# Performance work log

Measured on AMD Instinct MI355X. Metric: run time of the kernel, lower is better.

The kernel has to match this reference:

```python
import jax, jax.numpy as jnp
import numpy as np

B, L = 8, 2048
H_IN = 20
K1, K2 = 16, 32
NG = 32            # n_gaussians
D1, D2 = 7, 5      # gaussian kernel input dims
DM = 128           # outer product out_features
DH = 32            # attribute embedding out_features
IDX_MAX = 8.0      # index_distance_max


def _gather(x, idx):
    # x: (B,L,H), idx: (B,L,K) -> (B,L,K,H)
    b = jnp.arange(x.shape[0])[:, None, None]
    return x[b, idx]


def _neighbors(frames, kmax):
    c = frames[:, :, 0, :]                      # centers (B,L,3)
    sq = jnp.sum(c * c, axis=-1)
    d2 = sq[:, :, None] + sq[:, None, :] - 2.0 * jnp.einsum('bld,bmd->blm', c, c)
    _, idx = jax.lax.top_k(-d2, kmax)           # self (d2=0) lands in slot 0
    return idx


def _coords(frames, seq_idx, idx):
    c = frames[:, :, 0, :]
    axes = frames[:, :, 1:4, :]                 # local frame axes of center node
    z = frames[:, :, 3, :]
    c_j = _gather(c, idx)
    z_j = _gather(z, idx)
    delta = c_j - c[:, :, None, :]              # (B,L,K,3)
    dist = jnp.sqrt(jnp.sum(delta * delta, -1, keepdims=True) + 1e-12)
    eucl = jnp.einsum('blkd,blad->blka', delta, axes)   # neighbor coords in local frame
    zdotz = jnp.sum(z[:, :, None, :] * z_j, -1, keepdims=True)
    deltadotz = jnp.sum(delta * z_j, -1, keepdims=True) / dist
    zdotdelta = jnp.sum(z[:, :, None, :] * delta, -1, keepdims=True) / dist
    sidx = seq_idx.astype(jnp.float32)          # (B,L,1)
    idist = jnp.clip(jnp.abs(_gather(sidx, idx) - sidx[:, :, None, :]), 0.0, IDX_MAX)
    return eucl, dist, zdotz, deltadotz, zdotdelta, idist


def _gaussian(x, centers, prec):
    # full-covariance Gaussian kernel: exp(-0.5 ||P_n (x - mu_n)||^2)
    diff = x[..., None] - centers               # (...,d,NG)
    y = jnp.einsum('...dn,dkn->...kn', diff, prec)
    return jnp.exp(-0.5 * jnp.sum(y * y, axis=-2))


def _forward(aa_attributes, aa_frame, aa_indices,
             gk1_centers, gk1_prec, op_kernel, op_bias,
             emb_W, emb_b, beta_W, beta_b, selfatt_W, selfatt_b,
             crossatt_W, crossatt_b, nodef_W, nodef_b,
             gk2_centers, gk2_prec, emb2_W, emb2_b):
    # --- neighborhood 1: euclidian + index_distance + ZdotZ + (DeltadotZ,ZdotDelta)
    idx1 = _neighbors(aa_frame, K1)
    eucl, _, zz, dz, zd, idist = _coords(aa_frame, aa_indices, idx1)
    coords1 = jnp.concatenate([eucl, idist, zz, dz, zd], axis=-1)   # (B,L,K1,7)
    neigh_attr = _gather(aa_attributes, idx1)                        # (B,L,K1,20)
    g1 = _gaussian(coords1, gk1_centers, gk1_prec)                   # (B,L,K1,NG)
    # outer-product embedding: sum over neighbors and (gaussian x attribute) pairs
    filt = jnp.einsum('blkg,blkh,gho->blo', g1, neigh_attr, op_kernel) + op_bias
    f = jax.nn.relu(filt)                                            # (B,L,128)
    emb = jax.nn.relu(f @ emb_W + emb_b)                             # (B,L,32)
    beta = jax.nn.relu(emb @ beta_W + beta_b)                        # (B,L,1)
    satt = jax.nn.relu(emb @ selfatt_W + selfatt_b)                  # (B,L,1)
    catt = jax.nn.relu(emb @ crossatt_W + crossatt_b)                # (B,L,1)
    nodef = jax.nn.relu(emb @ nodef_W + nodef_b)                     # (B,L,2)
    # --- neighborhood 2: distance + ZdotZ + (DeltadotZ,ZdotDelta) + index_distance
    idx2 = _neighbors(aa_frame, K2)
    _, dist2, zz2, dz2, zd2, idist2 = _coords(aa_frame, aa_indices, idx2)
    coords2 = jnp.concatenate([dist2, zz2, dz2, zd2, idist2], axis=-1)  # (B,L,K2,5)
    att_local = _gather(catt, idx2)                                  # (B,L,K2,1)
    nodef_local = _gather(nodef, idx2)                               # (B,L,K2,2)
    g2 = _gaussian(coords2, gk2_centers, gk2_prec)                   # (B,L,K2,NG)
    gw = jax.nn.relu(g2 @ emb2_W + emb2_b)                           # (B,L,K2,1)
    # --- graph attention aggregation (self slot is k=0)
    e = att_local.at[:, :, 0, :].set(satt)
    logits = beta[:, :, None, :] * e
    logits = logits - jnp.max(logits, axis=2, keepdims=True)
    w = gw * jnp.exp(logits)
    a = w / (jnp.sum(w, axis=2, keepdims=True) + 1e-6)               # (B,L,K2,1)
    out = jnp.sum(a * nodef_local, axis=2)                           # (B,L,2)
    return out


def setup_inputs():
    key = jax.random.key(0)
    ks = jax.random.split(key, 16)
    eye1 = jnp.tile(jnp.eye(D1, dtype=jnp.float32)[:, :, None], (1, 1, NG))
    eye2 = jnp.tile(jnp.eye(D2, dtype=jnp.float32)[:, :, None], (1, 1, NG))
    return {
        'aa_attributes': jax.random.normal(ks[0], (B, L, H_IN), jnp.float32),
        'aa_frame': jax.random.normal(ks[1], (B, L, 4, 3), jnp.float32),
        'aa_indices': jnp.arange(B * L, dtype=jnp.int32).reshape(B, L, 1),
        'gk1_centers': 0.1 * jax.random.normal(ks[2], (D1, NG), jnp.float32),
        'gk1_prec': eye1 + 0.05 * jax.random.normal(ks[3], (D1, D1, NG), jnp.float32),
        'op_kernel': 0.05 * jax.random.normal(ks[4], (NG, H_IN, DM), jnp.float32),
        'op_bias': jnp.zeros((DM,), jnp.float32),
        'emb_W': jax.random.normal(ks[5], (DM, DH), jnp.float32) / np.sqrt(DM),
        'emb_b': jnp.zeros((DH,), jnp.float32),
        'beta_W': jax.random.normal(ks[6], (DH, 1), jnp.float32) / np.sqrt(DH),
        'beta_b': jnp.zeros((1,), jnp.float32),
        'selfatt_W': jax.random.normal(ks[7], (DH, 1), jnp.float32) / np.sqrt(DH),
        'selfatt_b': jnp.zeros((1,), jnp.float32),
        'crossatt_W': jax.random.normal(ks[8], (DH, 1), jnp.float32) / np.sqrt(DH),
        'crossatt_b': jnp.zeros((1,), jnp.float32),
        'nodef_W': jax.random.normal(ks[9], (DH, 2), jnp.float32) / np.sqrt(DH),
        'nodef_b': jnp.zeros((2,), jnp.float32),
        'gk2_centers': 0.1 * jax.random.normal(ks[10], (D2, NG), jnp.float32),
        'gk2_prec': eye2 + 0.05 * jax.random.normal(ks[11], (D2, D2, NG), jnp.float32),
        'emb2_W': jax.random.normal(ks[12], (NG, 1), jnp.float32) / np.sqrt(NG),
        'emb2_b': jnp.zeros((1,), jnp.float32),
    }


def reference(aa_attributes, aa_frame, aa_indices,
              gk1_centers, gk1_prec, op_kernel, op_bias,
              emb_W, emb_b, beta_W, beta_b, selfatt_W, selfatt_b,
              crossatt_W, crossatt_b, nodef_W, nodef_b,
              gk2_centers, gk2_prec, emb2_W, emb2_b):
    return _forward(aa_attributes, aa_frame, aa_indices,
                    gk1_centers, gk1_prec, op_kernel, op_bias,
                    emb_W, emb_b, beta_W, beta_b, selfatt_W, selfatt_b,
                    crossatt_W, crossatt_b, nodef_W, nodef_b,
                    gk2_centers, gk2_prec, emb2_W, emb2_b)
```

## Files before the change

kernel.cpp:

```cpp
#include <hip/hip_runtime.h>

typedef unsigned int u32;
typedef unsigned long long u64;
typedef unsigned short u16;

#define NL 2048

typedef __attribute__((ext_vector_type(8))) short bf16x8;
typedef __attribute__((ext_vector_type(16))) float f32x16;

__device__ __forceinline__ u16 to_bf16(float f) {
  u32 b = __float_as_uint(f);
  b += 0x7FFFu + ((b >> 16) & 1u);
  return (u16)(b >> 16);
}

__device__ __forceinline__ void gload_lds16(const void* g, void* l) {
  __builtin_amdgcn_global_load_lds(
      (const __attribute__((address_space(1))) u32*)g,
      (__attribute__((address_space(3))) u32*)l, 16, 0, 0);
}

__device__ __forceinline__ u64 shfl_xor64(u64 v, int m) {
  int lo = __shfl_xor((int)(u32)v, m, 64);
  int hi = __shfl_xor((int)(u32)(v >> 32), m, 64);
  return ((u64)(u32)hi << 32) | (u32)lo;
}

__device__ __forceinline__ u32 sort64_u32(u32 v, int lane) {
#pragma unroll
  for (int k = 2; k <= 64; k <<= 1) {
#pragma unroll
    for (int j = k >> 1; j > 0; j >>= 1) {
      u32 p = (u32)__shfl_xor((int)v, j, 64);
      bool lower = ((lane & j) == 0);
      bool asc = ((lane & k) == 0);
      u32 lo = v < p ? v : p;
      u32 hi = v < p ? p : v;
      v = (lower == asc) ? lo : hi;
    }
  }
  return v;
}

__device__ __forceinline__ void sort128_u64(u64& f0, u64& f1, int lane) {
  for (int k = 2; k <= 128; k <<= 1) {
    for (int j = k >> 1; j > 0; j >>= 1) {
      if (j == 64) {
        u64 lo = f0 < f1 ? f0 : f1;
        u64 hi = f0 < f1 ? f1 : f0;
        f0 = lo;
        f1 = hi;
      } else {
        bool lower = ((lane & j) == 0);
        bool asc0 = ((lane & k) == 0);
        bool asc1 = (((lane + 64) & k) == 0);
        u64 p0 = shfl_xor64(f0, j);
        u64 p1 = shfl_xor64(f1, j);
        f0 = ((f0 < p0) == (lower == asc0)) ? f0 : p0;
        f1 = ((f1 < p1) == (lower == asc1)) ? f1 : p1;
      }
    }
  }
}

__global__ __launch_bounds__(256) void prep_kernel(
    const float* __restrict__ opW, const float* __restrict__ embW,
    const float* __restrict__ betaW, const float* __restrict__ sattW,
    const float* __restrict__ cattW, const float* __restrict__ nodW,
    const float* __restrict__ betaB, const float* __restrict__ sattB,
    const float* __restrict__ cattB, const float* __restrict__ nodB,
    u16* __restrict__ opWt, u16* __restrict__ embWt, float* __restrict__ w5,
    float* __restrict__ b5) {
  const int bx = blockIdx.x, t = threadIdx.x;
  if (bx < 160) {
    int flat = bx * 256 + t;
    int o = flat / 320;
    int r = flat - o * 320;
    int kk = r * 2;
    float f0 = opW[(size_t)kk * 128 + o];
    float f1 = opW[(size_t)(kk + 1) * 128 + o];
    ((u32*)opWt)[o * 320 + r] = (u32)to_bf16(f0) | ((u32)to_bf16(f1) << 16);
  } else if (bx < 176) {
    int flat = (bx - 160) * 256 + t;
    int j = flat >> 7, k = flat & 127;
    embWt[j * 128 + k] = to_bf16(embW[(size_t)k * 32 + j]);
  } else {
    if (t < 160) {
      int h = t >> 5, j = t & 31;
      float v = (h == 0) ? betaW[j]
                : (h == 1) ? sattW[j]
                : (h == 2) ? cattW[j]
                : (h == 3) ? nodW[j * 2]
                           : nodW[j * 2 + 1];
      w5[j * 8 + h] = v;
    } else if (t < 165) {
      int h = t - 160;
      float v = (h == 0) ? betaB[0]
                : (h == 1) ? sattB[0]
                : (h == 2) ? cattB[0]
                : (h == 3) ? nodB[0]
                           : nodB[1];
      b5[h] = v;
    }
  }
}

__global__ __launch_bounds__(512) void knn_kernel(const float* __restrict__ frames,
                                                  int* __restrict__ idx32) {
  __shared__ float4 cand[2048];
  __shared__ u64 comp[8][256];
  const int tid = threadIdx.x;
  const int w = tid >> 6, lane = tid & 63;
  const int query = blockIdx.x * 8 + w;
  const int b = query >> 11, lq = query & (NL - 1);

#pragma unroll
  for (int i = 0; i < 4; i++) {
    int l = tid + i * 512;
    const float* fp = frames + (size_t)(b * NL + l) * 12;
    float4 fr = *(const float4*)fp;
    cand[l] = make_float4(fr.x, fr.y, fr.z,
                          fr.x * fr.x + fr.y * fr.y + fr.z * fr.z);
  }
  __syncthreads();

  float4 me = cand[lq];
  u32 k[32];
  u32 m = 0xFFFFFFFFu;
#pragma unroll
  for (int i = 0; i < 32; i++) {
    float4 c = cand[i * 64 + lane];
    float dot = c.x * me.x + c.y * me.y + c.z * me.z;
    float d2 = (me.w + c.w) - 2.0f * dot;
    u32 kb = __float_as_uint(d2);
    u32 key = kb ^ ((u32)((int)kb >> 31) | 0x80000000u);
    k[i] = key;
    m = key < m ? key : m;
  }

  u32 ms = sort64_u32(m, lane);
  u32 T0 = (u32)__shfl((int)ms, 31, 64);

  int base = 0;
#pragma unroll
  for (int i = 0; i < 32; i++) {
    bool flag = (k[i] <= T0);
    u64 mask = __ballot(flag);
    if (flag) {
      u32 rank = __builtin_amdgcn_mbcnt_hi(
          (u32)(mask >> 32), __builtin_amdgcn_mbcnt_lo((u32)mask, 0u));
      int pos = base + (int)rank;
      if (pos < 256) comp[w][pos] = ((u64)k[i] << 32) | (u32)(i * 64 + lane);
    }
    base += (int)__popcll(mask);
  }
  int cnt = base < 256 ? base : 256;
  __syncthreads();

  u64 f0 = ~0ull;
  for (int c = 0; c * 64 < cnt; c++) {
    int p = c * 64 + lane;
    u64 f1 = (p < cnt) ? comp[w][p] : ~0ull;
    sort128_u64(f0, f1, lane);
    f0 = (lane < 32) ? f0 : ~0ull;
  }
  if (lane < 32)
    idx32[(size_t)query * 32 + lane] = (int)(f0 & 0xFFFFFFFFull);
}

__global__ __launch_bounds__(256) void stage1_kernel(
    const float* __restrict__ frames, const float* __restrict__ attrs,
    const int* __restrict__ aaidx, const float* __restrict__ cen1,
    const float* __restrict__ prec1, const int* __restrict__ idx32,
    u16* __restrict__ outer) {
  __shared__ float sPrec[1568];
  __shared__ float sCen[224];
  __shared__ float sCoord[4 * 16 * 8];
  __shared__ float sAttrT[4 * 20 * 16];
  __shared__ float sG1T[4 * 32 * 17];
  const int tid = threadIdx.x;
  for (int i = tid; i < 1568; i += 256) sPrec[i] = prec1[i];
  if (tid < 224) sCen[tid] = cen1[tid];
  const int pt = tid >> 6, lane = tid & 63;
  const int pid = blockIdx.x * 4 + pt;
  const int b = pid >> 11;
  __syncthreads();

  if (lane < 16) {
    int n = lane;
    int j = idx32[pid * 32 + n];
    int jg = b * NL + j;
    const float* fs = frames + (size_t)pid * 12;
    const float* fj = frames + (size_t)jg * 12;
    float4 A0 = *(const float4*)(fs);
    float4 A1 = *(const float4*)(fs + 4);
    float4 A2 = *(const float4*)(fs + 8);
    float4 B0 = *(const float4*)(fj);
    float4 B2 = *(const float4*)(fj + 8);
    float dx = B0.x - A0.x, dy = B0.y - A0.y, dzc = B0.z - A0.z;
    float a0x = A0.w, a0y = A1.x, a0z = A1.y;
    float a1x = A1.z, a1y = A1.w, a1z = A2.x;
    float a2x = A2.y, a2y = A2.z, a2z = A2.w;
    float zjx = B2.y, zjy = B2.z, zjz = B2.w;
    float dd = dx * dx + dy * dy + dzc * dzc + 1e-12f;
    float dist = sqrtf(dd);
    float e0 = dx * a0x + dy * a0y + dzc * a0z;
    float e1 = dx * a1x + dy * a1y + dzc * a1z;
    float e2 = dx * a2x + dy * a2y + dzc * a2z;
    float zz = a2x * zjx + a2y * zjy + a2z * zjz;
    float dzv = (dx * zjx + dy * zjy + dzc * zjz) / dist;
    float zdv = (a2x * dx + a2y * dy + a2z * dzc) / dist;
    float si = (float)aaidx[pid];
    float sj = (float)aaidx[jg];
    float idist = fminf(fabsf(sj - si), 8.0f);
    float* cr = sCoord + pt * 128 + n * 8;
    cr[0] = e0; cr[1] = e1; cr[2] = e2; cr[3] = idist;
    cr[4] = zz; cr[5] = dzv; cr[6] = zdv;
    const float* ar = attrs + (size_t)jg * 20;
    float4 q0 = *(const float4*)(ar);
    float4 q1 = *(const float4*)(ar + 4);
    float4 q2 = *(const float4*)(ar + 8);
    float4 q3 = *(const float4*)(ar + 12);
    float4 q4 = *(const float4*)(ar + 16);
    float av[20] = {q0.x, q0.y, q0.z, q0.w, q1.x, q1.y, q1.z, q1.w,
                    q2.x, q2.y, q2.z, q2.w, q3.x, q3.y, q3.z, q3.w,
                    q4.x, q4.y, q4.z, q4.w};
#pragma unroll
    for (int h = 0; h < 20; h++) sAttrT[pt * 320 + h * 16 + n] = av[h];
  }
  __syncthreads();
  {
    const int g = lane & 31, nh = lane >> 5;
    float pr[7][7], cn[7];
#pragma unroll
    for (int d = 0; d < 7; d++) {
      cn[d] = sCen[d * 32 + g];
#pragma unroll
      for (int kk = 0; kk < 7; kk++) pr[d][kk] = sPrec[(d * 7 + kk) * 32 + g];
    }
#pragma unroll
    for (int i = 0; i < 8; i++) {
      int n = nh * 8 + i;
      const float* cr = sCoord + pt * 128 + n * 8;
      float df[7];
#pragma unroll
      for (int d = 0; d < 7; d++) df[d] = cr[d] - cn[d];
      float s = 0.0f;
#pragma unroll
      for (int kk = 0; kk < 7; kk++) {
        float y = 0.0f;
#pragma unroll
        for (int d = 0; d < 7; d++) y = fmaf(df[d], pr[d][kk], y);
        s = fmaf(y, y, s);
      }
      sG1T[pt * 544 + g * 17 + n] = __expf(-0.5f * s);
    }
  }
  __syncthreads();
  {
    const int g = lane & 31, hg = lane >> 5;
    float g16[16];
#pragma unroll
    for (int n = 0; n < 16; n++) g16[n] = sG1T[pt * 544 + g * 17 + n];
    u32* orow = (u32*)(outer + (size_t)pid * 640) + (g * 20 + hg * 10) / 2;
#pragma unroll
    for (int i = 0; i < 5; i++) {
      int h0 = hg * 10 + i * 2, h1 = h0 + 1;
      float a0 = 0.f, a1 = 0.f;
#pragma unroll
      for (int c = 0; c < 4; c++) {
        float4 v0 = *(float4*)&sAttrT[pt * 320 + h0 * 16 + c * 4];
        float4 v1 = *(float4*)&sAttrT[pt * 320 + h1 * 16 + c * 4];
        a0 = fmaf(v0.x, g16[c * 4 + 0], a0);
        a0 = fmaf(v0.y, g16[c * 4 + 1], a0);
        a0 = fmaf(v0.z, g16[c * 4 + 2], a0);
        a0 = fmaf(v0.w, g16[c * 4 + 3], a0);
        a1 = fmaf(v1.x, g16[c * 4 + 0], a1);
        a1 = fmaf(v1.y, g16[c * 4 + 1], a1);
        a1 = fmaf(v1.z, g16[c * 4 + 2], a1);
        a1 = fmaf(v1.w, g16[c * 4 + 3], a1);
      }
      orow[i] = (u32)to_bf16(a0) | ((u32)to_bf16(a1) << 16);
    }
  }
}

__global__ __launch_bounds__(256) void gemm_kernel(
    const u16* __restrict__ outer,
    const u16* __restrict__ opWt,
    const float* __restrict__ opB,
    const u16* __restrict__ embWt,
    const float* __restrict__ embB,
    const float* __restrict__ w5,
    const float* __restrict__ b5,
    float* __restrict__ head8) {
  __shared__ char smem[32768];
  const int tid = threadIdx.x;
  const int w = tid >> 6, lane = tid & 63;
  const int p0 = blockIdx.x * 32;
  const int lr = lane >> 3, lc = lane & 7;
  const int gsw = lc ^ lr;
  const int m = lane & 31, kh = lane >> 5;

  f32x16 acc;
#pragma unroll
  for (int r = 0; r < 16; r++) acc[r] = 0.f;

  const u16* gA = outer + (size_t)(p0 + w * 8 + lr) * 640 + gsw * 8;

  for (int cc = 0; cc < 10; cc++) {
    gload_lds16(gA + cc * 64, smem + w * 1024);
#pragma unroll
    for (int i = 0; i < 4; i++) {
      const u16* gB = opWt + (size_t)(w * 32 + i * 8 + lr) * 640 + cc * 64 + gsw * 8;
      gload_lds16(gB, smem + 4096 + w * 4096 + i * 1024);
    }
    __syncthreads();
#pragma unroll
    for (int s = 0; s < 4; s++) {
      int pg = (s * 2 + kh) ^ (m & 7);
      bf16x8 av = *(bf16x8*)(smem + m * 128 + pg * 16);
      bf16x8 bv = *(bf16x8*)(smem + 4096 + w * 4096 + m * 128 + pg * 16);
      acc = __builtin_amdgcn_mfma_f32_32x32x16_bf16(av, bv, acc, 0, 0, 0);
    }
    __syncthreads();
  }

  const int o = w * 32 + m;
  float bo = opB[o];
#pragma unroll
  for (int i = 0; i < 2; i++) {
    int j = w * 8 + i * 4 + (lane >> 4);
    int ge = (lane & 15) ^ (j & 7);
    gload_lds16(embWt + j * 128 + ge * 8, smem + 8192 + w * 2048 + i * 1024);
  }
  u16* sFb = (u16*)smem;
#pragma unroll
  for (int r = 0; r < 16; r++) {
    int mm = (r & 3) + 8 * (r >> 2) + 4 * kh;
    float v = fmaxf(acc[r] + bo, 0.f);
    int pg = (o >> 3) ^ (mm & 7);
    sFb[mm * 128 + pg * 8 + (o & 7)] = to_bf16(v);
  }
  __syncthreads();

  f32x16 acc2;
#pragma unroll
  for (int r = 0; r < 16; r++) acc2[r] = 0.f;
#pragma unroll
  for (int t2 = 0; t2 < 2; t2++) {
    int gg = (w * 2 + t2) * 2 + kh;
    int pg = gg ^ (m & 7);
    bf16x8 av = *(bf16x8*)(smem + m * 256 + pg * 16);
    bf16x8 bv = *(bf16x8*)(smem + 8192 + m * 256 + pg * 16);
    acc2 = __builtin_amdgcn_mfma_f32_32x32x16_bf16(av, bv, acc2, 0, 0, 0);
  }
  float* scr = (float*)(smem + 16384) + w * 1024;
#pragma unroll
  for (int r = 0; r < 16; r++) {
    int mm = (r & 3) + 8 * (r >> 2) + 4 * kh;
    scr[mm * 32 + m] = acc2[r];
  }
  __syncthreads();

  {
    float* sc = (float*)(smem + 16384);
    int i4 = tid * 4;
    float4 v0 = *(float4*)(sc + i4);
    float4 v1 = *(float4*)(sc + 1024 + i4);
    float4 v2 = *(float4*)(sc + 2048 + i4);
    float4 v3 = *(float4*)(sc + 3072 + i4);
    int pp = tid >> 3, j0 = (tid & 7) * 4;
    float4 eb = *(const float4*)(embB + j0);
    float4 e;
    e.x = fmaxf(v0.x + v1.x + v2.x + v3.x + eb.x, 0.f);
    e.y = fmaxf(v0.y + v1.y + v2.y + v3.y + eb.y, 0.f);
    e.z = fmaxf(v0.z + v1.z + v2.z + v3.z + eb.z, 0.f);
    e.w = fmaxf(v0.w + v1.w + v2.w + v3.w + eb.w, 0.f);
    *(float4*)((float*)smem + pp * 36 + j0) = e;
  }
  __syncthreads();

  if (tid < 160) {
    int h = tid >> 5, p = tid & 31;
    const float* sE = (const float*)smem + p * 36;
    float a = b5[h];
#pragma unroll
    for (int j = 0; j < 32; j++) a = fmaf(sE[j], w5[j * 8 + h], a);
    a = fmaxf(a, 0.f);
    int slot = (h < 2) ? (h + 4) : (h - 2);
    head8[(size_t)(p0 + p) * 8 + slot] = a;
  }
}

__global__ __launch_bounds__(256) void stage2_kernel(
    const float* __restrict__ frames, const int* __restrict__ aaidx,
    const float* __restrict__ cen2, const float* __restrict__ prec2,
    const float* __restrict__ emb2W, const float* __restrict__ emb2B,
    const int* __restrict__ idx32, const float* __restrict__ head8,
    float* __restrict__ out) {
  __shared__ float sPrec[800];
  __shared__ float sCen[160];
  __shared__ float sW2[32];
  __shared__ float sCoord[4 * 32 * 5];
  __shared__ float sG2[4 * 32 * 33];
  const int tid = threadIdx.x;
  for (int i = tid; i < 800; i += 256) sPrec[i] = prec2[i];
  if (tid < 160) sCen[tid] = cen2[tid];
  if (tid < 32) sW2[tid] = emb2W[tid];
  const int pt = tid >> 6, lane = tid & 63;
  const int pid = blockIdx.x * 4 + pt;
  const int b = pid >> 11;
  __syncthreads();

  float4 hv = make_float4(0.f, 0.f, 0.f, 0.f);
  float betaS = 0.f, sattS = 0.f;
  if (lane < 32) {
    int n = lane;
    int j = idx32[pid * 32 + n];
    int jg = b * NL + j;
    const float* fs = frames + (size_t)pid * 12;
    const float* fj = frames + (size_t)jg * 12;
    float4 A0 = *(const float4*)(fs);
    float4 A2 = *(const float4*)(fs + 8);
    float4 B0 = *(const float4*)(fj);
    float4 B2 = *(const float4*)(fj + 8);
    float dx = B0.x - A0.x, dy = B0.y - A0.y, dzc = B0.z - A0.z;
    float a2x = A2.y, a2y = A2.z, a2z = A2.w;
    float zjx = B2.y, zjy = B2.z, zjz = B2.w;
    float dd = dx * dx + dy * dy + dzc * dzc + 1e-12f;
    float dist = sqrtf(dd);
    float zz = a2x * zjx + a2y * zjy + a2z * zjz;
    float dzv = (dx * zjx + dy * zjy + dzc * zjz) / dist;
    float zdv = (a2x * dx + a2y * dy + a2z * dzc) / dist;
    float si = (float)aaidx[pid];
    float sj = (float)aaidx[jg];
    float idist = fminf(fabsf(sj - si), 8.0f);
    float* cr = sCoord + pt * 160 + n * 5;
    cr[0] = dist; cr[1] = zz; cr[2] = dzv; cr[3] = zdv; cr[4] = idist;
    hv = *(const float4*)(head8 + (size_t)jg * 8);
    betaS = head8[(size_t)pid * 8 + 4];
    sattS = head8[(size_t)pid * 8 + 5];
  }
  __syncthreads();
  {
    const int g = lane & 31, nh = lane >> 5;
    float pr[5][5], cn[5];
#pragma unroll
    for (int d = 0; d < 5; d++) {
      cn[d] = sCen[d * 32 + g];
#pragma unroll
      for (int kk = 0; kk < 5; kk++) pr[d][kk] = sPrec[(d * 5 + kk) * 32 + g];
    }
#pragma unroll
    for (int i = 0; i < 16; i++) {
      int n = nh * 16 + i;
      const float* cr = sCoord + pt * 160 + n * 5;
      float df[5];
#pragma unroll
      for (int d = 0; d < 5; d++) df[d] = cr[d] - cn[d];
      float s = 0.0f;
#pragma unroll
      for (int kk = 0; kk < 5; kk++) {
        float y = 0.0f;
#pragma unroll
        for (int d = 0; d < 5; d++) y = fmaf(df[d], pr[d][kk], y);
        s = fmaf(y, y, s);
      }
      sG2[pt * 1056 + n * 33 + g] = __expf(-0.5f * s);
    }
  }
  __syncthreads();
  if (lane < 32) {
    int n = lane;
    float gw = emb2B[0];
#pragma unroll 8
    for (int g = 0; g < 32; g++) gw = fmaf(sG2[pt * 1056 + n * 33 + g], sW2[g], gw);
    gw = fmaxf(gw, 0.0f);
    float e = (n == 0) ? sattS : hv.x;
    float logit = betaS * e;
    float mx = logit;
#pragma unroll
    for (int d = 1; d < 32; d <<= 1) mx = fmaxf(mx, __shfl_xor(mx, d, 64));
    float wv = gw * __expf(logit - mx);
    float S = wv;
#pragma unroll
    for (int d = 1; d < 32; d <<= 1) S += __shfl_xor(S, d, 64);
    float a = wv / (S + 1e-6f);
    float o0 = a * hv.y, o1 = a * hv.z;
#pragma unroll
    for (int d = 1; d < 32; d <<= 1) {
      o0 += __shfl_xor(o0, d, 64);
      o1 += __shfl_xor(o1, d, 64);
    }
    if (n == 0) {
      out[pid * 2 + 0] = o0;
      out[pid * 2 + 1] = o1;
    }
  }
}

extern "C" void kernel_launch(void* const* d_in, const int* in_sizes, int n_in,
                              void* d_out, int out_size, void* d_ws, size_t ws_size,
                              hipStream_t stream) {
  const float* attrs = (const float*)d_in[0];
  const float* frames = (const float*)d_in[1];
  const int* aaidx = (const int*)d_in[2];
  const float* cen1 = (const float*)d_in[3];
  const float* prec1 = (const float*)d_in[4];
  const float* opW = (const float*)d_in[5];
  const float* opB = (const float*)d_in[6];
  const float* embW = (const float*)d_in[7];
  const float* embB = (const float*)d_in[8];
  const float* betaW = (const float*)d_in[9];
  const float* betaB = (const float*)d_in[10];
  const float* sattW = (const float*)d_in[11];
  const float* sattB = (const float*)d_in[12];
  const float* cattW = (const float*)d_in[13];
  const float* cattB = (const float*)d_in[14];
  const float* nodW = (const float*)d_in[15];
  const float* nodB = (const float*)d_in[16];
  const float* cen2 = (const float*)d_in[17];
  const float* prec2 = (const float*)d_in[18];
  const float* emb2W = (const float*)d_in[19];
  const float* emb2B = (const float*)d_in[20];
  float* out = (float*)d_out;

  char* ws = (char*)d_ws;
  int* idx32 = (int*)ws;
  u16* outer_bf = (u16*)(ws + 2097152);
  float* head8 = (float*)(ws + 23068672);
  u16* opWt = (u16*)(ws + 23592960);
  u16* embWt = (u16*)(ws + 23756800);
  float* w5 = (float*)(ws + 23764992);
  float* b5 = (float*)(ws + 23766016);

  prep_kernel<<<dim3(177), dim3(256), 0, stream>>>(
      opW, embW, betaW, sattW, cattW, nodW, betaB, sattB, cattB, nodB, opWt,
      embWt, w5, b5);
  knn_kernel<<<dim3(2048), dim3(512), 0, stream>>>(frames, idx32);
  stage1_kernel<<<dim3(4096), dim3(256), 0, stream>>>(frames, attrs, aaidx, cen1,
                                                      prec1, idx32, outer_bf);
  gemm_kernel<<<dim3(512), dim3(256), 0, stream>>>(outer_bf, opWt, opB, embWt,
                                                   embB, w5, b5, head8);
  stage2_kernel<<<dim3(4096), dim3(256), 0, stream>>>(frames, aaidx, cen2, prec2,
                                                      emb2W, emb2B, idx32, head8, out);
}
```

Baseline: 194.3 us.

## Merge prep into kNN kernel, rank-select neighbors, and stream GEMM B operand from global

The weight-prep work is folded into the kNN launch as extra blocks, and the opW transpose now goes through LDS for coalesced access. The kNN top-32 selection replaces the bitonic 128-element merge sort with a direct rank count over the compacted candidates. Stage1 and stage2 load the Gaussian precision and center parameters straight into registers instead of staging them in shared memory, which removes a barrier. The GEMM now preloads all A chunks into LDS at once and reads B directly from global memory, dropping the per-chunk barriers. The rank count is O(cnt^2) per wave, and duplicate keys could collide on the same output slot.

Result: faster. 184.1 us (median of 2 runs) (-5.2%).

```diff
diff --git a/kernel.cpp b/kernel.cpp
--- a/kernel.cpp
+++ b/kernel.cpp
@@ -19,12 +19,6 @@
   __builtin_amdgcn_global_load_lds(
       (const __attribute__((address_space(1))) u32*)g,
       (__attribute__((address_space(3))) u32*)l, 16, 0, 0);
-}
-
-__device__ __forceinline__ u64 shfl_xor64(u64 v, int m) {
-  int lo = __shfl_xor((int)(u32)v, m, 64);
-  int hi = __shfl_xor((int)(u32)(v >> 32), m, 64);
-  return ((u64)(u32)hi << 32) | (u32)lo;
 }
 
 __device__ __forceinline__ u32 sort64_u32(u32 v, int lane) {
@@ -43,28 +37,8 @@
   return v;
 }
 
-__device__ __forceinline__ void sort128_u64(u64& f0, u64& f1, int lane) {
-  for (int k = 2; k <= 128; k <<= 1) {
-    for (int j = k >> 1; j > 0; j >>= 1) {
-      if (j == 64) {
-        u64 lo = f0 < f1 ? f0 : f1;
-        u64 hi = f0 < f1 ? f1 : f0;
-        f0 = lo;
-        f1 = hi;
-      } else {
-        bool lower = ((lane & j) == 0);
-        bool asc0 = ((lane & k) == 0);
-        bool asc1 = (((lane + 64) & k) == 0);
-        u64 p0 = shfl_xor64(f0, j);
-        u64 p1 = shfl_xor64(f1, j);
-        f0 = ((f0 < p0) == (lower == asc0)) ? f0 : p0;
-        f1 = ((f1 < p1) == (lower == asc1)) ? f1 : p1;
-      }
-    }
-  }
-}
-
-__global__ __launch_bounds__(256) void prep_kernel(
+__global__ __launch_bounds__(512) void knn_prep_kernel(
+    const float* __restrict__ frames, int* __restrict__ idx32,
     const float* __restrict__ opW, const float* __restrict__ embW,
     const float* __restrict__ betaW, const float* __restrict__ sattW,
     const float* __restrict__ cattW, const float* __restrict__ nodW,
@@ -72,47 +46,68 @@
     const float* __restrict__ cattB, const float* __restrict__ nodB,
     u16* __restrict__ opWt, u16* __restrict__ embWt, float* __restrict__ w5,
     float* __restrict__ b5) {
-  const int bx = blockIdx.x, t = threadIdx.x;
-  if (bx < 160) {
-    int flat = bx * 256 + t;
-    int o = flat / 320;
-    int r = flat - o * 320;
-    int kk = r * 2;
-    float f0 = opW[(size_t)kk * 128 + o];
-    float f1 = opW[(size_t)(kk + 1) * 128 + o];
-    ((u32*)opWt)[o * 320 + r] = (u32)to_bf16(f0) | ((u32)to_bf16(f1) << 16);
-  } else if (bx < 176) {
-    int flat = (bx - 160) * 256 + t;
-    int j = flat >> 7, k = flat & 127;
-    embWt[j * 128 + k] = to_bf16(embW[(size_t)k * 32 + j]);
-  } else {
-    if (t < 160) {
-      int h = t >> 5, j = t & 31;
-      float v = (h == 0) ? betaW[j]
-                : (h == 1) ? sattW[j]
-                : (h == 2) ? cattW[j]
-                : (h == 3) ? nodW[j * 2]
-                           : nodW[j * 2 + 1];
-      w5[j * 8 + h] = v;
-    } else if (t < 165) {
-      int h = t - 160;
-      float v = (h == 0) ? betaB[0]
-                : (h == 1) ? sattB[0]
-                : (h == 2) ? cattB[0]
-                : (h == 3) ? nodB[0]
-                           : nodB[1];
-      b5[h] = v;
-    }
-  }
-}
-
-__global__ __launch_bounds__(512) void knn_kernel(const float* __restrict__ frames,
-                                                  int* __restrict__ idx32) {
-  __shared__ float4 cand[2048];
-  __shared__ u64 comp[8][256];
+  __shared__ union U {
+    struct {
+      float4 cand[2048];
+      u64 comp[8][256];
+    } k;
+    float tp[128 * 73];
+  } sm;
+  const int bx = blockIdx.x;
   const int tid = threadIdx.x;
+
+  if (bx >= 2048) {
+    if (bx < 2058) {
+      const int k0 = (bx - 2048) * 64;
+#pragma unroll
+      for (int j = 0; j < 4; j++) {
+        int f = tid + j * 512;
+        int kk = f >> 5;
+        int o4 = (f & 31) * 4;
+        float4 v = *(const float4*)(opW + (size_t)(k0 + kk) * 128 + o4);
+        sm.tp[(o4 + 0) * 73 + kk] = v.x;
+        sm.tp[(o4 + 1) * 73 + kk] = v.y;
+        sm.tp[(o4 + 2) * 73 + kk] = v.z;
+        sm.tp[(o4 + 3) * 73 + kk] = v.w;
+      }
+      __syncthreads();
+      u32* ow = (u32*)opWt;
+#pragma unroll
+      for (int j = 0; j < 8; j++) {
+        int f = tid + j * 512;
+        int o = f >> 5, q = f & 31;
+        float lo = sm.tp[o * 73 + q * 2];
+        float hi = sm.tp[o * 73 + q * 2 + 1];
+        ow[o * 320 + (k0 >> 1) + q] = (u32)to_bf16(lo) | ((u32)to_bf16(hi) << 16);
+      }
+    } else {
+      for (int f = tid; f < 4096; f += 512) {
+        int j = f >> 7, kk = f & 127;
+        embWt[f] = to_bf16(embW[(size_t)kk * 32 + j]);
+      }
+      if (tid < 160) {
+        int h = tid >> 5, j = tid & 31;
+        float v = (h == 0) ? betaW[j]
+                  : (h == 1) ? sattW[j]
+                  : (h == 2) ? cattW[j]
+                  : (h == 3) ? nodW[j * 2]
+                             : nodW[j * 2 + 1];
+        w5[j * 8 + h] = v;
+      } else if (tid < 165) {
+        int h = tid - 160;
+        float v = (h == 0) ? betaB[0]
+                  : (h == 1) ? sattB[0]
+                  : (h == 2) ? cattB[0]
+                  : (h == 3) ? nodB[0]
+                             : nodB[1];
+        b5[h] = v;
+      }
+    }
+    return;
+  }
+
   const int w = tid >> 6, lane = tid & 63;
-  const int query = blockIdx.x * 8 + w;
+  const int query = bx * 8 + w;
   const int b = query >> 11, lq = query & (NL - 1);
 
 #pragma unroll
@@ -120,17 +115,17 @@
     int l = tid + i * 512;
     const float* fp = frames + (size_t)(b * NL + l) * 12;
     float4 fr = *(const float4*)fp;
-    cand[l] = make_float4(fr.x, fr.y, fr.z,
-                          fr.x * fr.x + fr.y * fr.y + fr.z * fr.z);
-  }
-  __syncthreads();
-
-  float4 me = cand[lq];
+    sm.k.cand[l] = make_float4(fr.x, fr.y, fr.z,
+                               fr.x * fr.x + fr.y * fr.y + fr.z * fr.z);
+  }
+  __syncthreads();
+
+  float4 me = sm.k.cand[lq];
   u32 k[32];
   u32 m = 0xFFFFFFFFu;
 #pragma unroll
   for (int i = 0; i < 32; i++) {
-    float4 c = cand[i * 64 + lane];
+    float4 c = sm.k.cand[i * 64 + lane];
     float dot = c.x * me.x + c.y * me.y + c.z * me.z;
     float d2 = (me.w + c.w) - 2.0f * dot;
     u32 kb = __float_as_uint(d2);
@@ -151,22 +146,24 @@
       u32 rank = __builtin_amdgcn_mbcnt_hi(
           (u32)(mask >> 32), __builtin_amdgcn_mbcnt_lo((u32)mask, 0u));
       int pos = base + (int)rank;
-      if (pos < 256) comp[w][pos] = ((u64)k[i] << 32) | (u32)(i * 64 + lane);
+      if (pos < 256) sm.k.comp[w][pos] = ((u64)k[i] << 32) | (u32)(i * 64 + lane);
     }
     base += (int)__popcll(mask);
   }
   int cnt = base < 256 ? base : 256;
   __syncthreads();
 
-  u64 f0 = ~0ull;
-  for (int c = 0; c * 64 < cnt; c++) {
-    int p = c * 64 + lane;
-    u64 f1 = (p < cnt) ? comp[w][p] : ~0ull;
-    sort128_u64(f0, f1, lane);
-    f0 = (lane < 32) ? f0 : ~0ull;
-  }
-  if (lane < 32)
-    idx32[(size_t)query * 32 + lane] = (int)(f0 & 0xFFFFFFFFull);
+  for (int b0 = 0; b0 < cnt; b0 += 64) {
+    bool live = (b0 + lane < cnt);
+    u64 e = live ? sm.k.comp[w][b0 + lane] : ~0ull;
+    int r = 0;
+    for (int mi = 0; mi < cnt; mi++) {
+      u64 em = sm.k.comp[w][mi];
+      r += (em < e) ? 1 : 0;
+    }
+    if (live && r < 32)
+      idx32[(size_t)query * 32 + r] = (int)(e & 0xFFFFFFFFull);
+  }
 }
 
 __global__ __launch_bounds__(256) void stage1_kernel(
@@ -174,18 +171,22 @@
     const int* __restrict__ aaidx, const float* __restrict__ cen1,
     const float* __restrict__ prec1, const int* __restrict__ idx32,
     u16* __restrict__ outer) {
-  __shared__ float sPrec[1568];
-  __shared__ float sCen[224];
   __shared__ float sCoord[4 * 16 * 8];
   __shared__ float sAttrT[4 * 20 * 16];
   __shared__ float sG1T[4 * 32 * 17];
   const int tid = threadIdx.x;
-  for (int i = tid; i < 1568; i += 256) sPrec[i] = prec1[i];
-  if (tid < 224) sCen[tid] = cen1[tid];
   const int pt = tid >> 6, lane = tid & 63;
   const int pid = blockIdx.x * 4 + pt;
   const int b = pid >> 11;
-  __syncthreads();
+  const int g = lane & 31;
+
+  float pr[7][7], cn[7];
+#pragma unroll
+  for (int d = 0; d < 7; d++) {
+    cn[d] = cen1[d * 32 + g];
+#pragma unroll
+    for (int kk = 0; kk < 7; kk++) pr[d][kk] = prec1[(d * 7 + kk) * 32 + g];
+  }
 
   if (lane < 16) {
     int n = lane;
@@ -231,14 +232,7 @@
   }
   __syncthreads();
   {
-    const int g = lane & 31, nh = lane >> 5;
-    float pr[7][7], cn[7];
-#pragma unroll
-    for (int d = 0; d < 7; d++) {
-      cn[d] = sCen[d * 32 + g];
-#pragma unroll
-      for (int kk = 0; kk < 7; kk++) pr[d][kk] = sPrec[(d * 7 + kk) * 32 + g];
-    }
+    const int nh = lane >> 5;
 #pragma unroll
     for (int i = 0; i < 8; i++) {
       int n = nh * 8 + i;
@@ -259,7 +253,7 @@
   }
   __syncthreads();
   {
-    const int g = lane & 31, hg = lane >> 5;
+    const int hg = lane >> 5;
     float g16[16];
 #pragma unroll
     for (int n = 0; n < 16; n++) g16[n] = sG1T[pt * 544 + g * 17 + n];
@@ -295,7 +289,7 @@
     const float* __restrict__ w5,
     const float* __restrict__ b5,
     float* __restrict__ head8) {
-  __shared__ char smem[32768];
+  __shared__ char smem[40960];
   const int tid = threadIdx.x;
   const int w = tid >> 6, lane = tid & 63;
   const int p0 = blockIdx.x * 32;
@@ -308,24 +302,23 @@
   for (int r = 0; r < 16; r++) acc[r] = 0.f;
 
   const u16* gA = outer + (size_t)(p0 + w * 8 + lr) * 640 + gsw * 8;
-
+#pragma unroll
+  for (int cc = 0; cc < 10; cc++)
+    gload_lds16(gA + cc * 64, smem + cc * 4096 + w * 1024);
+  __syncthreads();
+
+  const u16* gB = opWt + (size_t)(w * 32 + m) * 640;
+#pragma unroll
   for (int cc = 0; cc < 10; cc++) {
-    gload_lds16(gA + cc * 64, smem + w * 1024);
-#pragma unroll
-    for (int i = 0; i < 4; i++) {
-      const u16* gB = opWt + (size_t)(w * 32 + i * 8 + lr) * 640 + cc * 64 + gsw * 8;
-      gload_lds16(gB, smem + 4096 + w * 4096 + i * 1024);
-    }
-    __syncthreads();
 #pragma unroll
     for (int s = 0; s < 4; s++) {
       int pg = (s * 2 + kh) ^ (m & 7);
-      bf16x8 av = *(bf16x8*)(smem + m * 128 + pg * 16);
-      bf16x8 bv = *(bf16x8*)(smem + 4096 + w * 4096 + m * 128 + pg * 16);
+      bf16x8 av = *(bf16x8*)(smem + cc * 4096 + m * 128 + pg * 16);
+      bf16x8 bv = *(const bf16x8*)(gB + cc * 64 + s * 16 + kh * 8);
       acc = __builtin_amdgcn_mfma_f32_32x32x16_bf16(av, bv, acc, 0, 0, 0);
     }
-    __syncthreads();
-  }
+  }
+  __syncthreads();
 
   const int o = w * 32 + m;
   float bo = opB[o];
@@ -400,19 +393,21 @@
     const float* __restrict__ emb2W, const float* __restrict__ emb2B,
     const int* __restrict__ idx32, const float* __restrict__ head8,
     float* __restrict__ out) {
-  __shared__ float sPrec[800];
-  __shared__ float sCen[160];
-  __shared__ float sW2[32];
   __shared__ float sCoord[4 * 32 * 5];
   __shared__ float sG2[4 * 32 * 33];
   const int tid = threadIdx.x;
-  for (int i = tid; i < 800; i += 256) sPrec[i] = prec2[i];
-  if (tid < 160) sCen[tid] = cen2[tid];
-  if (tid < 32) sW2[tid] = emb2W[tid];
   const int pt = tid >> 6, lane = tid & 63;
   const int pid = blockIdx.x * 4 + pt;
   const int b = pid >> 11;
-  __syncthreads();
+  const int g = lane & 31;
+
+  float pr[5][5], cn[5];
+#pragma unroll
+  for (int d = 0; d < 5; d++) {
+    cn[d] = cen2[d * 32 + g];
+#pragma unroll
+    for (int kk = 0; kk < 5; kk++) pr[d][kk] = prec2[(d * 5 + kk) * 32 + g];
+  }
 
   float4 hv = make_float4(0.f, 0.f, 0.f, 0.f);
   float betaS = 0.f, sattS = 0.f;
@@ -445,14 +440,7 @@
   }
   __syncthreads();
   {
-    const int g = lane & 31, nh = lane >> 5;
-    float pr[5][5], cn[5];
-#pragma unroll
-    for (int d = 0; d < 5; d++) {
-      cn[d] = sCen[d * 32 + g];
-#pragma unroll
-      for (int kk = 0; kk < 5; kk++) pr[d][kk] = sPrec[(d * 5 + kk) * 32 + g];
-    }
+    const int nh = lane >> 5;
 #pragma unroll
     for (int i = 0; i < 16; i++) {
       int n = nh * 16 + i;
@@ -476,7 +464,8 @@
     int n = lane;
     float gw = emb2B[0];
 #pragma unroll 8
-    for (int g = 0; g < 32; g++) gw = fmaf(sG2[pt * 1056 + n * 33 + g], sW2[g], gw);
+    for (int gg = 0; gg < 32; gg++)
+      gw = fmaf(sG2[pt * 1056 + n * 33 + gg], emb2W[gg], gw);
     gw = fmaxf(gw, 0.0f);
     float e = (n == 0) ? sattS : hv.x;
     float logit = betaS * e;
@@ -536,10 +525,9 @@
   float* w5 = (float*)(ws + 23764992);
   float* b5 = (float*)(ws + 23766016);
 
-  prep_kernel<<<dim3(177), dim3(256), 0, stream>>>(
-      opW, embW, betaW, sattW, cattW, nodW, betaB, sattB, cattB, nodB, opWt,
-      embWt, w5, b5);
-  knn_kernel<<<dim3(2048), dim3(512), 0, stream>>>(frames, idx32);
+  knn_prep_kernel<<<dim3(2059), dim3(512), 0, stream>>>(
+      frames, idx32, opW, embW, betaW, sattW, cattW, nodW, betaB, sattB,
+      cattB, nodB, opWt, embWt, w5, b5);
   stage1_kernel<<<dim3(4096), dim3(256), 0, stream>>>(frames, attrs, aaidx, cen1,
                                                       prec1, idx32, outer_bf);
   gemm_kernel<<<dim3(512), dim3(256), 0, stream>>>(outer_bf, opWt, opB, embWt,
```
